# Optimization experiments

Hardware: AMD Instinct MI355X
Metric: run time of the kernel (lower is better)

The kernel has to match this reference:

```python
import jax, jax.numpy as jnp
import numpy as np


def setup_inputs() -> dict:
    key = jax.random.key(0)
    k1, k2, k3 = jax.random.split(key, 3)
    B, L, S, H, E, D = 2, 512, 512, 8, 32, 64
    queries = jax.random.normal(k1, (B, L, H, E), dtype=jnp.float32)
    keys = jax.random.normal(k2, (B, S, H, E), dtype=jnp.float32)
    values = jax.random.normal(k3, (B, S, H, D), dtype=jnp.float32)
    v = jnp.ones((E,), dtype=jnp.float32)
    attn_mask_add = jnp.zeros((L, S), dtype=jnp.float32)
    key_lengths_add = jnp.zeros((B, S), dtype=jnp.float32)
    return {
        "queries": queries,
        "keys": keys,
        "values": values,
        "v": v,
        "attn_mask_add": attn_mask_add,
        "key_lengths_add": key_lengths_add,
    }


def reference(queries, keys, values, v, attn_mask_add, key_lengths_add):
    # Additive (Bahdanau) attention.
    # queries: (B,L,H,E), keys: (B,S,H,E), values: (B,S,H,D)
    # Broadcast add -> tanh -> contract with v: (B,L,S,H,E) -> (B,H,L,S)
    feat = jnp.tanh(queries[:, :, None, :, :] + keys[:, None, :, :, :])  # (B,L,S,H,E)
    scores = jnp.einsum("blshe,e->bhls", feat, v)  # (B,H,L,S)
    scores = scores + attn_mask_add[None, None, :, :]          # (L,S) attn mask
    scores = scores + key_lengths_add[:, None, None, :]        # (B,S) key-length mask
    A = jax.nn.softmax(scores, axis=-1)  # (B,H,L,S); dropout is identity (p=0 / eval)
    V = jnp.einsum("bhls,bshd->blhd", A, values)  # (B,L,H,D)
    return V
```

## Files before the change

### kernel.cpp

```cpp
#include <hip/hip_runtime.h>


#define BB 2
#define LL 512
#define SS 512
#define HH 8
#define EE 32
#define DD 64

#define WS_EK_OFF 0
#define WS_EQ_OFF (2u * 1024u * 1024u)
#define WS_VT_OFF (4u * 1024u * 1024u)

typedef __attribute__((ext_vector_type(8))) short bf16x8;
typedef __attribute__((ext_vector_type(4))) float f32x4;
typedef __attribute__((ext_vector_type(4))) unsigned u32x4;

__device__ __forceinline__ unsigned short f2bf(float f) {
    unsigned u = __float_as_uint(f);
    u += 0x7FFFu + ((u >> 16) & 1u);
    return (unsigned short)(u >> 16);
}
__device__ __forceinline__ float fast_exp2(float x) {
#if __has_builtin(__builtin_amdgcn_exp2f)
    return __builtin_amdgcn_exp2f(x);
#else
    return exp2f(x);
#endif
}
__device__ __forceinline__ float fast_rcp(float x) {
    return __builtin_amdgcn_rcpf(x);
}
__device__ __forceinline__ float bcastf(float x) {
    return __int_as_float(__builtin_amdgcn_readfirstlane(__float_as_int(x)));
}

#define SCV 2.885390081777927f

__global__ __launch_bounds__(256) void prep_kernel(
    const float* __restrict__ q, const float* __restrict__ k,
    const float* __restrict__ vals, float* __restrict__ ws)
{
    unsigned gid = blockIdx.x * 256 + threadIdx.x;
    if (gid < 65536u) {
        unsigned i  = gid;
        unsigned s  = i & 511u;
        unsigned e4 = (i >> 9) & 7u;
        unsigned h  = (i >> 12) & 7u;
        unsigned b  = i >> 15;
        float4 kv = *(const float4*)(k + (((size_t)b * SS + s) * HH + h) * EE + e4 * 4);
        float4 ev = make_float4(fast_exp2(SCV * kv.x), fast_exp2(SCV * kv.y),
                                fast_exp2(SCV * kv.z), fast_exp2(SCV * kv.w));
        ((float4*)(ws + WS_EK_OFF / 4))[i] = ev;
    } else if (gid < 131072u) {
        unsigned i = gid - 65536u;
        float4 qv = ((const float4*)q)[i];
        float4 ev = make_float4(fast_exp2(SCV * qv.x), fast_exp2(SCV * qv.y),
                                fast_exp2(SCV * qv.z), fast_exp2(SCV * qv.w));
        ((float4*)(ws + WS_EQ_OFF / 4))[i] = ev;
    } else {
        unsigned p   = gid - 131072u;
        unsigned sp8 = p & 63u;
        unsigned d   = (p >> 6) & 63u;
        unsigned h   = (p >> 12) & 7u;
        unsigned b   = p >> 15;
        unsigned s0  = sp8 * 8u;
        const float* vb = vals + (((size_t)b * SS + s0) * HH + h) * DD + d;
        u32x4 pk;
        #pragma unroll
        for (int j = 0; j < 4; j++) {
            float f0 = vb[(size_t)(2 * j) * (HH * DD)];
            float f1 = vb[(size_t)(2 * j + 1) * (HH * DD)];
            pk[j] = (unsigned)f2bf(f0) | ((unsigned)f2bf(f1) << 16);
        }
        u32x4* vt4 = (u32x4*)((char*)ws + WS_VT_OFF);
        vt4[((((size_t)b * HH + h) * DD + d) * SS + s0) / 8] = pk;
    }
}

__global__ __launch_bounds__(256) void addattn_kernel(
    const float* __restrict__ ws_ekf,
    const float* __restrict__ ws_eqf,
    const unsigned short* __restrict__ ws_vt,
    const float* __restrict__ vvec,
    const float* __restrict__ mask,
    const float* __restrict__ klen,
    float* __restrict__ out)
{
    __shared__ unsigned short sAb[8][SS];

    const int tid  = threadIdx.x;
    const int w    = tid >> 6;
    const int lane = tid & 63;
    const int bh   = blockIdx.x >> 6;
    const int lblk = blockIdx.x & 63;
    const int b    = bh >> 3;
    const int h    = bh & 7;
    const int l0   = lblk * 8;
    const int lw   = l0 + 2 * w;

    float eq0[EE], eq1[EE], v2s[EE];
    {
        const float* q0 = ws_eqf + (((size_t)b * LL + lw) * HH + h) * EE;
        const float* q1 = q0 + HH * EE;
        #pragma unroll
        for (int e = 0; e < EE; e += 4) {
            float4 t0 = *(const float4*)(q0 + e);
            float4 t1 = *(const float4*)(q1 + e);
            eq0[e] = bcastf(t0.x); eq0[e+1] = bcastf(t0.y);
            eq0[e+2] = bcastf(t0.z); eq0[e+3] = bcastf(t0.w);
            eq1[e] = bcastf(t1.x); eq1[e+1] = bcastf(t1.y);
            eq1[e+2] = bcastf(t1.z); eq1[e+3] = bcastf(t1.w);
        }
        const float4* vr = (const float4*)vvec;
        #pragma unroll
        for (int e4 = 0; e4 < EE / 4; e4++) {
            float4 t = vr[e4];
            v2s[e4*4]   = -2.f * t.x; v2s[e4*4+1] = -2.f * t.y;
            v2s[e4*4+2] = -2.f * t.z; v2s[e4*4+3] = -2.f * t.w;
        }
    }

    float sc[2][SS / 64];
    const float4* ekp = (const float4*)ws_ekf + (size_t)(b * HH + h) * (8 * SS);

    float4 cur[4], nxt[4];
    #pragma unroll
    for (int e4 = 0; e4 < 4; e4++) cur[e4] = ekp[e4 * SS + lane];

    for (int i = 0; i < SS / 64; i++) {
        const int s  = lane + i * 64;
        const int sn = lane + ((i + 1) & 7) * 64;
        float a0[4] = {0.f, 0.f, 0.f, 0.f};
        float a1[4] = {0.f, 0.f, 0.f, 0.f};

        #define COMPC(IDX, comp)                                              \
        {                                                                     \
            float p0 = __builtin_fmaf(eq0[IDX], comp, 1.f);                   \
            float p1 = __builtin_fmaf(eq1[IDX], comp, 1.f);                   \
            a0[(IDX) & 3] = __builtin_fmaf(v2s[IDX], fast_rcp(p0), a0[(IDX) & 3]); \
            a1[(IDX) & 3] = __builtin_fmaf(v2s[IDX], fast_rcp(p1), a1[(IDX) & 3]); \
        }
        #define COMP4(E4, kv)                                                 \
        {                                                                     \
            COMPC(4 * (E4) + 0, kv.x) COMPC(4 * (E4) + 1, kv.y)               \
            COMPC(4 * (E4) + 2, kv.z) COMPC(4 * (E4) + 3, kv.w)               \
        }

        #pragma unroll
        for (int e4 = 0; e4 < 4; e4++) nxt[e4] = ekp[(e4 + 4) * SS + s];
        #pragma unroll
        for (int e4 = 0; e4 < 4; e4++) { float4 kv = cur[e4]; COMP4(e4, kv) }
        #pragma unroll
        for (int e4 = 0; e4 < 4; e4++) cur[e4] = ekp[e4 * SS + sn];
        #pragma unroll
        for (int e4 = 0; e4 < 4; e4++) { float4 kv = nxt[e4]; COMP4(e4 + 4, kv) }

        sc[0][i] = (a0[0] + a0[1]) + (a0[2] + a0[3]);
        sc[1][i] = (a1[0] + a1[1]) + (a1[2] + a1[3]);
        #undef COMP4
        #undef COMPC
    }

    {
        const float* kl = klen + (size_t)b * SS;
        float klv[SS / 64];
        #pragma unroll
        for (int i = 0; i < SS / 64; i++) klv[i] = kl[lane + i * 64];

        #pragma unroll
        for (int r = 0; r < 2; r++) {
            const float* mrow = mask + (size_t)(lw + r) * SS;
            float mx = -1e30f;
            #pragma unroll
            for (int i = 0; i < SS / 64; i++) {
                sc[r][i] += mrow[lane + i * 64] + klv[i];
                mx = fmaxf(mx, sc[r][i]);
            }
            #pragma unroll
            for (int off = 1; off < 64; off <<= 1) mx = fmaxf(mx, __shfl_xor(mx, off, 64));
            float ssum = 0.f;
            #pragma unroll
            for (int i = 0; i < SS / 64; i++) {
                sc[r][i] = __expf(sc[r][i] - mx);
                ssum += sc[r][i];
            }
            #pragma unroll
            for (int off = 1; off < 64; off <<= 1) ssum += __shfl_xor(ssum, off, 64);
            float inv = fast_rcp(ssum);
            const int row = 2 * w + r;
            const int fsw = (row * 5) & 7;
            #pragma unroll
            for (int i = 0; i < SS / 64; i++) {
                int col = lane + i * 64;
                int pos = (((col >> 3) ^ fsw) << 3) | (col & 7);
                sAb[row][pos] = f2bf(sc[r][i] * inv);
            }
        }
    }
    __syncthreads();

    const int am  = lane & 15;
    const int qd  = lane >> 4;
    const int dof = w * 16 + am;
    const int fam = (am * 5) & 7;
    const unsigned short* vt =
        ws_vt + (((size_t)b * HH + h) * DD + dof) * SS + qd * 8;
    f32x4 acc = {0.f, 0.f, 0.f, 0.f};
    bf16x8 bcur = *(const bf16x8*)vt;
    for (int c = 0; c < SS / 32; c++) {
        bf16x8 bnxt = bcur;
        if (c < SS / 32 - 1) bnxt = *(const bf16x8*)(vt + (c + 1) * 32);
        bf16x8 af = {0, 0, 0, 0, 0, 0, 0, 0};
        if (am < 8)
            af = *(const bf16x8*)&sAb[am][((c * 4 + qd) ^ fam) << 3];
        acc = __builtin_amdgcn_mfma_f32_16x16x32_bf16(af, bcur, acc, 0, 0, 0);
        bcur = bnxt;
    }
    if (qd < 2) {
        float* orow = out + (((size_t)b * LL + l0 + qd * 4) * HH + h) * DD + dof;
        #pragma unroll
        for (int r = 0; r < 4; r++)
            orow[(size_t)r * (HH * DD)] = acc[r];
    }
}

extern "C" void kernel_launch(void* const* d_in, const int* in_sizes, int n_in,
                              void* d_out, int out_size, void* d_ws, size_t ws_size,
                              hipStream_t stream) {
    const float* q    = (const float*)d_in[0];
    const float* k    = (const float*)d_in[1];
    const float* vals = (const float*)d_in[2];
    const float* vvec = (const float*)d_in[3];
    const float* mask = (const float*)d_in[4];
    const float* klen = (const float*)d_in[5];
    float* outp = (float*)d_out;

    float* ws = (float*)d_ws;
    prep_kernel<<<dim3(768), dim3(256), 0, stream>>>(q, k, vals, ws);

    const float* ws_ekf = (const float*)((char*)d_ws + WS_EK_OFF);
    const float* ws_eqf = (const float*)((char*)d_ws + WS_EQ_OFF);
    const unsigned short* ws_vt = (const unsigned short*)((char*)d_ws + WS_VT_OFF);
    addattn_kernel<<<dim3(BB * HH * (LL / 8)), dim3(256), 0, stream>>>(
        ws_ekf, ws_eqf, ws_vt, vvec, mask, klen, outp);
}
```

Measured before the change: 98.73 us.

## Store exp(k) as bf16, stage it in LDS, and pre-swizzle V fragments

The precomputed exp(k) table is stored as packed bf16 instead of fp32, which halves its footprint. Each block copies its head's table into shared memory once and reads it from there, replacing repeated global loads inside the score loop. The V transpose is rewritten in MFMA fragment order, so each lane in the PV loop does one contiguous 16-byte load. Rounding exp(k) to bf16 adds error to the tanh scores, and the extra LDS (32KB) may reduce occupancy.

```diff
diff --git a/kernel.cpp b/kernel.cpp
--- a/kernel.cpp
+++ b/kernel.cpp
@@ -42,51 +42,63 @@
     const float* __restrict__ vals, float* __restrict__ ws)
 {
     unsigned gid = blockIdx.x * 256 + threadIdx.x;
-    if (gid < 65536u) {
+    if (gid < 32768u) {
         unsigned i  = gid;
         unsigned s  = i & 511u;
-        unsigned e4 = (i >> 9) & 7u;
-        unsigned h  = (i >> 12) & 7u;
-        unsigned b  = i >> 15;
-        float4 kv = *(const float4*)(k + (((size_t)b * SS + s) * HH + h) * EE + e4 * 4);
-        float4 ev = make_float4(fast_exp2(SCV * kv.x), fast_exp2(SCV * kv.y),
-                                fast_exp2(SCV * kv.z), fast_exp2(SCV * kv.w));
-        ((float4*)(ws + WS_EK_OFF / 4))[i] = ev;
-    } else if (gid < 131072u) {
-        unsigned i = gid - 65536u;
+        unsigned e8 = (i >> 9) & 3u;
+        unsigned h  = (i >> 11) & 7u;
+        unsigned b  = i >> 14;
+        const float* kr = k + (((size_t)b * SS + s) * HH + h) * EE + e8 * 8;
+        float4 k0 = *(const float4*)kr;
+        float4 k1 = *(const float4*)(kr + 4);
+        u32x4 pk;
+        pk[0] = (unsigned)f2bf(fast_exp2(SCV * k0.x)) |
+                ((unsigned)f2bf(fast_exp2(SCV * k0.y)) << 16);
+        pk[1] = (unsigned)f2bf(fast_exp2(SCV * k0.z)) |
+                ((unsigned)f2bf(fast_exp2(SCV * k0.w)) << 16);
+        pk[2] = (unsigned)f2bf(fast_exp2(SCV * k1.x)) |
+                ((unsigned)f2bf(fast_exp2(SCV * k1.y)) << 16);
+        pk[3] = (unsigned)f2bf(fast_exp2(SCV * k1.z)) |
+                ((unsigned)f2bf(fast_exp2(SCV * k1.w)) << 16);
+        ((u32x4*)((char*)ws + WS_EK_OFF))[i] = pk;
+    } else if (gid < 98304u) {
+        unsigned i = gid - 32768u;
         float4 qv = ((const float4*)q)[i];
         float4 ev = make_float4(fast_exp2(SCV * qv.x), fast_exp2(SCV * qv.y),
                                 fast_exp2(SCV * qv.z), fast_exp2(SCV * qv.w));
         ((float4*)(ws + WS_EQ_OFF / 4))[i] = ev;
     } else {
-        unsigned p   = gid - 131072u;
-        unsigned sp8 = p & 63u;
-        unsigned d   = (p >> 6) & 63u;
-        unsigned h   = (p >> 12) & 7u;
-        unsigned b   = p >> 15;
-        unsigned s0  = sp8 * 8u;
+        unsigned i      = gid - 98304u;
+        unsigned lane   = i & 63u;
+        unsigned c      = (i >> 6) & 15u;
+        unsigned dchunk = (i >> 10) & 3u;
+        unsigned h      = (i >> 12) & 7u;
+        unsigned b      = i >> 15;
+        unsigned qd = lane >> 4, n = lane & 15;
+        unsigned d  = dchunk * 16 + n;
+        unsigned s0 = c * 32 + qd * 8;
         const float* vb = vals + (((size_t)b * SS + s0) * HH + h) * DD + d;
         u32x4 pk;
         #pragma unroll
-        for (int j = 0; j < 4; j++) {
-            float f0 = vb[(size_t)(2 * j) * (HH * DD)];
-            float f1 = vb[(size_t)(2 * j + 1) * (HH * DD)];
-            pk[j] = (unsigned)f2bf(f0) | ((unsigned)f2bf(f1) << 16);
-        }
-        u32x4* vt4 = (u32x4*)((char*)ws + WS_VT_OFF);
-        vt4[((((size_t)b * HH + h) * DD + d) * SS + s0) / 8] = pk;
+        for (int j2 = 0; j2 < 4; j2++) {
+            float f0 = vb[(size_t)(2 * j2) * (HH * DD)];
+            float f1 = vb[(size_t)(2 * j2 + 1) * (HH * DD)];
+            pk[j2] = (unsigned)f2bf(f0) | ((unsigned)f2bf(f1) << 16);
+        }
+        ((u32x4*)((char*)ws + WS_VT_OFF))[i] = pk;
     }
 }
 
 __global__ __launch_bounds__(256) void addattn_kernel(
-    const float* __restrict__ ws_ekf,
+    const u32x4* __restrict__ ws_ekb,
     const float* __restrict__ ws_eqf,
-    const unsigned short* __restrict__ ws_vt,
+    const bf16x8* __restrict__ ws_vtf,
     const float* __restrict__ vvec,
     const float* __restrict__ mask,
     const float* __restrict__ klen,
     float* __restrict__ out)
 {
+    __shared__ u32x4 sek[4 * SS];
     __shared__ unsigned short sAb[8][SS];
 
     const int tid  = threadIdx.x;
@@ -99,6 +111,13 @@
     const int l0   = lblk * 8;
     const int lw   = l0 + 2 * w;
 
+    {
+        const u32x4* esrc = ws_ekb + (size_t)(b * HH + h) * (4 * SS);
+        #pragma unroll
+        for (int t = 0; t < 8; t++)
+            sek[tid + t * 256] = esrc[tid + t * 256];
+    }
+
     float eq0[EE], eq1[EE], v2s[EE];
     {
         const float* q0 = ws_eqf + (((size_t)b * LL + lw) * HH + h) * EE;
@@ -120,46 +139,41 @@
             v2s[e4*4+2] = -2.f * t.z; v2s[e4*4+3] = -2.f * t.w;
         }
     }
+    __syncthreads();
 
     float sc[2][SS / 64];
-    const float4* ekp = (const float4*)ws_ekf + (size_t)(b * HH + h) * (8 * SS);
-
-    float4 cur[4], nxt[4];
-    #pragma unroll
-    for (int e4 = 0; e4 < 4; e4++) cur[e4] = ekp[e4 * SS + lane];
-
     for (int i = 0; i < SS / 64; i++) {
-        const int s  = lane + i * 64;
-        const int sn = lane + ((i + 1) & 7) * 64;
+        const int s = lane + i * 64;
+        u32x4 g0 = sek[s];
+        u32x4 g1 = sek[SS + s];
+        u32x4 g2 = sek[2 * SS + s];
+        u32x4 g3 = sek[3 * SS + s];
         float a0[4] = {0.f, 0.f, 0.f, 0.f};
         float a1[4] = {0.f, 0.f, 0.f, 0.f};
-
-        #define COMPC(IDX, comp)                                              \
+        #define ELEM(E, F)                                                    \
         {                                                                     \
-            float p0 = __builtin_fmaf(eq0[IDX], comp, 1.f);                   \
-            float p1 = __builtin_fmaf(eq1[IDX], comp, 1.f);                   \
-            a0[(IDX) & 3] = __builtin_fmaf(v2s[IDX], fast_rcp(p0), a0[(IDX) & 3]); \
-            a1[(IDX) & 3] = __builtin_fmaf(v2s[IDX], fast_rcp(p1), a1[(IDX) & 3]); \
-        }
-        #define COMP4(E4, kv)                                                 \
+            float p0 = __builtin_fmaf(eq0[E], F, 1.f);                        \
+            float p1 = __builtin_fmaf(eq1[E], F, 1.f);                        \
+            a0[(E) & 3] = __builtin_fmaf(v2s[E], fast_rcp(p0), a0[(E) & 3]);  \
+            a1[(E) & 3] = __builtin_fmaf(v2s[E], fast_rcp(p1), a1[(E) & 3]);  \
+        }
+        #define PAIR(u, E)                                                    \
         {                                                                     \
-            COMPC(4 * (E4) + 0, kv.x) COMPC(4 * (E4) + 1, kv.y)               \
-            COMPC(4 * (E4) + 2, kv.z) COMPC(4 * (E4) + 3, kv.w)               \
-        }
-
-        #pragma unroll
-        for (int e4 = 0; e4 < 4; e4++) nxt[e4] = ekp[(e4 + 4) * SS + s];
-        #pragma unroll
-        for (int e4 = 0; e4 < 4; e4++) { float4 kv = cur[e4]; COMP4(e4, kv) }
-        #pragma unroll
-        for (int e4 = 0; e4 < 4; e4++) cur[e4] = ekp[e4 * SS + sn];
-        #pragma unroll
-        for (int e4 = 0; e4 < 4; e4++) { float4 kv = nxt[e4]; COMP4(e4 + 4, kv) }
-
+            float flo = __uint_as_float((u) << 16);                           \
+            float fhi = __uint_as_float((u) & 0xffff0000u);                   \
+            ELEM(E, flo) ELEM((E) + 1, fhi)                                   \
+        }
+        #define GRP(g, base)                                                  \
+        {                                                                     \
+            PAIR(g[0], (base) + 0) PAIR(g[1], (base) + 2)                     \
+            PAIR(g[2], (base) + 4) PAIR(g[3], (base) + 6)                     \
+        }
+        GRP(g0, 0) GRP(g1, 8) GRP(g2, 16) GRP(g3, 24)
+        #undef GRP
+        #undef PAIR
+        #undef ELEM
         sc[0][i] = (a0[0] + a0[1]) + (a0[2] + a0[3]);
         sc[1][i] = (a1[0] + a1[1]) + (a1[2] + a1[3]);
-        #undef COMP4
-        #undef COMPC
     }
 
     {
@@ -204,13 +218,13 @@
     const int qd  = lane >> 4;
     const int dof = w * 16 + am;
     const int fam = (am * 5) & 7;
-    const unsigned short* vt =
-        ws_vt + (((size_t)b * HH + h) * DD + dof) * SS + qd * 8;
+    const bf16x8* vf =
+        ws_vtf + ((size_t)((b * HH + h) * 4 + w) * 16) * 64 + lane;
     f32x4 acc = {0.f, 0.f, 0.f, 0.f};
-    bf16x8 bcur = *(const bf16x8*)vt;
+    bf16x8 bcur = vf[0];
     for (int c = 0; c < SS / 32; c++) {
         bf16x8 bnxt = bcur;
-        if (c < SS / 32 - 1) bnxt = *(const bf16x8*)(vt + (c + 1) * 32);
+        if (c < SS / 32 - 1) bnxt = vf[(c + 1) * 64];
         bf16x8 af = {0, 0, 0, 0, 0, 0, 0, 0};
         if (am < 8)
             af = *(const bf16x8*)&sAb[am][((c * 4 + qd) ^ fam) << 3];
@@ -237,11 +251,11 @@
     float* outp = (float*)d_out;
 
     float* ws = (float*)d_ws;
-    prep_kernel<<<dim3(768), dim3(256), 0, stream>>>(q, k, vals, ws);
-
-    const float* ws_ekf = (const float*)((char*)d_ws + WS_EK_OFF);
+    prep_kernel<<<dim3(640), dim3(256), 0, stream>>>(q, k, vals, ws);
+
+    const u32x4* ws_ekb = (const u32x4*)((char*)d_ws + WS_EK_OFF);
     const float* ws_eqf = (const float*)((char*)d_ws + WS_EQ_OFF);
-    const unsigned short* ws_vt = (const unsigned short*)((char*)d_ws + WS_VT_OFF);
+    const bf16x8* ws_vtf = (const bf16x8*)((char*)d_ws + WS_VT_OFF);
     addattn_kernel<<<dim3(BB * HH * (LL / 8)), dim3(256), 0, stream>>>(
-        ws_ekf, ws_eqf, ws_vt, vvec, mask, klen, outp);
-}
+        ws_ekb, ws_eqf, ws_vtf, vvec, mask, klen, outp);
+}
```

Result: faster. 93.75 us (-5.0%).
